# Kernel tuning notes

Hardware: AMD Instinct MI355X
Metric: run time of the kernel (lower is better)

Reference implementation:

```python
import jax, jax.numpy as jnp
import numpy as np

ATTN_C = 32
HEADS = 8
MSA_C = 256


def setup_inputs() -> dict:
    key = jax.random.key(0)
    ks = jax.random.split(key, 10)
    B, S, R, C = 1, 256, 384, MSA_C
    HC = ATTN_C * HEADS
    scale = 1.0 / np.sqrt(C)
    return {
        "msa_act": jax.random.normal(ks[0], (B, S, R, C), dtype=jnp.float32),
        "msa_mask": jnp.ones((B, S, R), dtype=jnp.float32),
        "ln_g": jnp.ones((C,), dtype=jnp.float32),
        "ln_b": jnp.zeros((C,), dtype=jnp.float32),
        "wq": jax.random.normal(ks[1], (C, HC), dtype=jnp.float32) * scale,
        "wk": jax.random.normal(ks[2], (C, HC), dtype=jnp.float32) * scale,
        "wv": jax.random.normal(ks[3], (C, HC), dtype=jnp.float32) * scale,
        "wg": jax.random.normal(ks[4], (C, HC), dtype=jnp.float32) * scale,
        "bg": jnp.zeros((HC,), dtype=jnp.float32),
        "wo": jax.random.normal(ks[5], (HC, C), dtype=jnp.float32) * (1.0 / np.sqrt(HC)),
        "bo": jnp.zeros((C,), dtype=jnp.float32),
    }


def _layernorm(x, g, b, eps=1e-5):
    mu = jnp.mean(x, axis=-1, keepdims=True)
    var = jnp.mean(jnp.square(x - mu), axis=-1, keepdims=True)
    return (x - mu) * jax.lax.rsqrt(var + eps) * g + b


def reference(msa_act, msa_mask, ln_g, ln_b, wq, wk, wv, wg, bg, wo, bo):
    H, AC = HEADS, ATTN_C
    # transpose: attend over sequence (column) axis
    x = jnp.swapaxes(msa_act, -2, -3)            # [b, R, S, C]
    mask = jnp.swapaxes(msa_mask, -1, -2)        # [b, R, S]
    bias = (1e9 * (mask - 1.0))[..., :, None, None, :]  # [b, R, 1, 1, S]
    x = _layernorm(x, ln_g, ln_b)
    shp = x.shape[:-1]
    gate = jax.nn.sigmoid((x @ wg + bg).reshape(*shp, H, AC))
    factor = 1.0 / np.sqrt(AC)
    q = (x @ wq).reshape(*shp, H, AC) * factor
    k = (x @ wk).reshape(*shp, H, AC)
    v = (x @ wv).reshape(*shp, H, AC)
    aff = jnp.einsum('brshc,brthc->brhst', q, k) + bias  # [b,R,H,S,S]
    w = jax.nn.softmax(aff, axis=-1)
    out = jnp.einsum('brhst,brthc->brshc', w, v) * gate  # [b,R,S,H,AC]
    out = out.reshape(*shp, H * AC) @ wo + bo            # [b,R,S,C]
    return jnp.swapaxes(out, -2, -3)                     # [b,S,R,C]
```

## Files before the change

kernel.cpp:

```cpp
#include <hip/hip_runtime.h>

#define S_DIM 256
#define R_DIM 384
#define C_DIM 256
#define H_DIM 8
#define AC_DIM 32
#define HC_DIM 256
#define M_DIM (S_DIM * R_DIM)

typedef __attribute__((ext_vector_type(8))) short short8;
typedef __attribute__((ext_vector_type(4))) float floatx4;

__device__ __forceinline__ unsigned short f2bf(float f) {
  unsigned u = __float_as_uint(f);
  u += 0x7FFFu + ((u >> 16) & 1u);
  return (unsigned short)(u >> 16);
}
__device__ __forceinline__ float bf2f(unsigned short s) {
  return __uint_as_float(((unsigned)s) << 16);
}
__device__ __forceinline__ unsigned packbf2(float a, float b) {
  return (unsigned)f2bf(a) | ((unsigned)f2bf(b) << 16);
}

#define GLD_LDS16(gp, lp)                                                      \
  __builtin_amdgcn_global_load_lds(                                            \
      (const __attribute__((address_space(1))) unsigned int*)(gp),             \
      (__attribute__((address_space(3))) unsigned int*)(lp), 16, 0, 0)

__global__ __launch_bounds__(256) void wcat_kernel(
    const float* __restrict__ wq, const float* __restrict__ wk,
    const float* __restrict__ wv, const float* __restrict__ wg,
    const float* __restrict__ wo, unsigned short* __restrict__ wt) {
  __shared__ float tile[64][65];
  const int n0 = blockIdx.x * 64;
  const int k0 = blockIdx.y * 64;
  const int wi = n0 >> 8;
  const float* src = (wi == 0) ? wq : (wi == 1) ? wk : (wi == 2) ? wv
                   : (wi == 3) ? wg : wo;
  const int col0 = n0 & 255;
  const int tx = threadIdx.x & 63;
  const int ty = threadIdx.x >> 6;
#pragma unroll
  for (int i = 0; i < 16; ++i) {
    int kl = ty + i * 4;
    tile[kl][tx] = src[(size_t)(k0 + kl) * 256 + col0 + tx];
  }
  __syncthreads();
#pragma unroll
  for (int i = 0; i < 16; ++i) {
    int nl = ty + i * 4;
    wt[(size_t)(n0 + nl) * 256 + k0 + tx] = f2bf(tile[tx][nl]);
  }
}

__global__ __launch_bounds__(256) void ln_kernel(
    const float* __restrict__ msa, const float* __restrict__ ln_g,
    const float* __restrict__ ln_b, unsigned short* __restrict__ xln) {
  const int p = blockIdx.x * 4 + (threadIdx.x >> 6);
  const int lane = threadIdx.x & 63;
  const float4 v = ((const float4*)(msa + (size_t)p * C_DIM))[lane];
  float s = v.x + v.y + v.z + v.w;
  float ss = v.x * v.x + v.y * v.y + v.z * v.z + v.w * v.w;
#pragma unroll
  for (int o = 1; o < 64; o <<= 1) {
    s += __shfl_xor(s, o);
    ss += __shfl_xor(ss, o);
  }
  const float mu = s * (1.0f / C_DIM);
  const float rstd = rsqrtf(ss * (1.0f / C_DIM) - mu * mu + 1e-5f);
  const float4 g = ((const float4*)ln_g)[lane];
  const float4 b = ((const float4*)ln_b)[lane];
  const int sq = p / R_DIM;
  const int r = p - sq * R_DIM;
  const size_t m = (size_t)r * S_DIM + sq;
  ushort4 o;
  o.x = f2bf((v.x - mu) * rstd * g.x + b.x);
  o.y = f2bf((v.y - mu) * rstd * g.y + b.y);
  o.z = f2bf((v.z - mu) * rstd * g.z + b.z);
  o.w = f2bf((v.w - mu) * rstd * g.w + b.w);
  *(ushort4*)(xln + m * C_DIM + lane * 4) = o;
}

#define EPI_S 136

__global__ __launch_bounds__(256, 3) void proj_kernel(
    const unsigned short* __restrict__ xln, const unsigned short* __restrict__ wt,
    const float* __restrict__ bg, unsigned short* __restrict__ q_ws,
    unsigned short* __restrict__ k_ws, unsigned short* __restrict__ v_ws,
    unsigned short* __restrict__ g_ws) {
  __shared__ __align__(16) unsigned short As[8 * 512];
  __shared__ __align__(16) unsigned short Bs[8 * 512];
  __shared__ __align__(16) unsigned short Epi[128 * EPI_S];

  const int bid = blockIdx.x;
  const int orig = (bid & 7) * 768 + (bid >> 3);
  const int n0 = (orig & 7) << 7;
  const int m0 = (orig >> 3) << 7;

  const int tid = threadIdx.x;
  const int wave = tid >> 6, lane = tid & 63;
  const int qd = lane >> 4, lm = lane & 15;
  const int wm = (wave & 1) * 64, wn = (wave >> 1) * 64;

  const int ga0 = wave * 2, ga1 = wave * 2 + 1;
  const unsigned short* agp0 = xln + (size_t)(m0 + ga0 * 16 + lm) * 256 + qd * 8;
  const unsigned short* agp1 = xln + (size_t)(m0 + ga1 * 16 + lm) * 256 + qd * 8;
  const unsigned short* bgp0 = wt + (size_t)(n0 + ga0 * 16 + lm) * 256 + qd * 8;
  const unsigned short* bgp1 = wt + (size_t)(n0 + ga1 * 16 + lm) * 256 + qd * 8;
  unsigned short* lA0 = &As[ga0 * 512];
  unsigned short* lA1 = &As[ga1 * 512];
  unsigned short* lB0 = &Bs[ga0 * 512];
  unsigned short* lB1 = &Bs[ga1 * 512];

  floatx4 acc[4][4];
#pragma unroll
  for (int i = 0; i < 4; ++i)
#pragma unroll
    for (int j = 0; j < 4; ++j) acc[i][j] = (floatx4){0.f, 0.f, 0.f, 0.f};

  for (int k0 = 0; k0 < 256; k0 += 32) {
    GLD_LDS16(agp0 + k0, lA0);
    GLD_LDS16(agp1 + k0, lA1);
    GLD_LDS16(bgp0 + k0, lB0);
    GLD_LDS16(bgp1 + k0, lB1);
    __syncthreads();
    short8 af[4], bf[4];
#pragma unroll
    for (int t = 0; t < 4; ++t) {
      af[t] = *(const short8*)((const char*)As + (size_t)(wm / 16 + t) * 1024 + lane * 16);
      bf[t] = *(const short8*)((const char*)Bs + (size_t)(wn / 16 + t) * 1024 + lane * 16);
    }
#pragma unroll
    for (int tm = 0; tm < 4; ++tm)
#pragma unroll
      for (int tn = 0; tn < 4; ++tn)
        acc[tm][tn] =
            __builtin_amdgcn_mfma_f32_16x16x32_bf16(af[tm], bf[tn], acc[tm][tn], 0, 0, 0);
    __syncthreads();
  }

  const int wi = n0 >> 8;
  const int cb = n0 & 255;
#pragma unroll
  for (int tm = 0; tm < 4; ++tm)
#pragma unroll
    for (int tn = 0; tn < 4; ++tn) {
      float bgv = 0.0f;
      if (wi == 3) bgv = bg[cb + wn + tn * 16 + lm];
#pragma unroll
      for (int rg = 0; rg < 4; ++rg) {
        const int lr = wm + tm * 16 + qd * 4 + rg;
        const int lc = wn + tn * 16 + lm;
        const float val = acc[tm][tn][rg];
        unsigned short o;
        if (wi == 0) o = f2bf(val * 0.17677669529663689f);
        else if (wi == 3) o = f2bf(1.0f / (1.0f + __expf(-(val + bgv))));
        else o = f2bf(val);
        Epi[lr * EPI_S + lc] = o;
      }
    }
  __syncthreads();
  unsigned short* dst = (wi == 0) ? q_ws : (wi == 1) ? k_ws
                      : (wi == 2) ? v_ws : g_ws;
#pragma unroll
  for (int p = 0; p < 8; ++p) {
    const int lr = (p >> 1) * 32 + (tid >> 3);
    const int lc = (p & 1) * 64 + (tid & 7) * 8;
    short8 v8 = *(const short8*)&Epi[lr * EPI_S + lc];
    *(short8*)(dst + (size_t)(m0 + lr) * 256 + cb + lc) = v8;
  }
}

#define PSTRIDE 40
#define VSTRIDE 264

__global__ __launch_bounds__(256) void attn_kernel(
    const unsigned short* __restrict__ q_ws, const unsigned short* __restrict__ k_ws,
    const unsigned short* __restrict__ v_ws, const unsigned short* __restrict__ g_ws,
    const float* __restrict__ mask, unsigned short* __restrict__ ctx_ws) {
  __shared__ __align__(16) unsigned short V_lds[32 * VSTRIDE];
  __shared__ __align__(16) unsigned short P_lds[4 * 16 * PSTRIDE];
  __shared__ float Bias[S_DIM];

  const int r = blockIdx.x;
  const int h = blockIdx.y;
  const int tid = threadIdx.x;
  const int wave = tid >> 6, lane = tid & 63;
  const int qd = lane >> 4, lm = lane & 15;
  const int qw = wave * 64;

  const size_t rS = (size_t)r * S_DIM;
  const int hb = h * AC_DIM;

  {
    const int s = tid;
    const unsigned short* vp = v_ws + (rS + s) * HC_DIM + hb;
    const int pos = (s & ~31) + ((s & 15) * 2) + ((s >> 4) & 1);
    uint4 u0 = *(const uint4*)(vp);
    uint4 u1 = *(const uint4*)(vp + 8);
    uint4 u2 = *(const uint4*)(vp + 16);
    uint4 u3 = *(const uint4*)(vp + 24);
    const unsigned w[16] = {u0.x, u0.y, u0.z, u0.w, u1.x, u1.y, u1.z, u1.w,
                            u2.x, u2.y, u2.z, u2.w, u3.x, u3.y, u3.z, u3.w};
#pragma unroll
    for (int d2 = 0; d2 < 16; ++d2) {
      V_lds[(d2 * 2 + 0) * VSTRIDE + pos] = (unsigned short)(w[d2] & 0xFFFF);
      V_lds[(d2 * 2 + 1) * VSTRIDE + pos] = (unsigned short)(w[d2] >> 16);
    }
    Bias[s] = 1e9f * (mask[(size_t)s * R_DIM + r] - 1.0f);
  }

  short8 qf[4];
#pragma unroll
  for (int qi = 0; qi < 4; ++qi)
    qf[qi] = *(const short8*)(q_ws + (rS + qw + qi * 16 + lm) * HC_DIM + hb + qd * 8);

  float m_st[4][4], l_st[4][4];
  floatx4 oacc[4][2];
#pragma unroll
  for (int qi = 0; qi < 4; ++qi) {
#pragma unroll
    for (int rg = 0; rg < 4; ++rg) {
      m_st[qi][rg] = -1e30f;
      l_st[qi][rg] = 0.0f;
    }
    oacc[qi][0] = (floatx4){0.f, 0.f, 0.f, 0.f};
    oacc[qi][1] = (floatx4){0.f, 0.f, 0.f, 0.f};
  }

  __syncthreads();

  unsigned short* Pw = &P_lds[wave * 16 * PSTRIDE];
  const floatx4 zero4 = (floatx4){0.f, 0.f, 0.f, 0.f};

  for (int ch = 0; ch < 8; ++ch) {
    const int kb = ch * 32;
    const float b0 = Bias[kb + lm];
    const float b1 = Bias[kb + 16 + lm];
    short8 kf0 = *(const short8*)(k_ws + (rS + kb + lm) * HC_DIM + hb + qd * 8);
    short8 kf1 = *(const short8*)(k_ws + (rS + kb + 16 + lm) * HC_DIM + hb + qd * 8);
    short8 vf0 = *(const short8*)&V_lds[lm * VSTRIDE + kb + qd * 8];
    short8 vf1 = *(const short8*)&V_lds[(16 + lm) * VSTRIDE + kb + qd * 8];

#pragma unroll
    for (int qi = 0; qi < 4; ++qi) {
      floatx4 s0 = __builtin_amdgcn_mfma_f32_16x16x32_bf16(qf[qi], kf0, zero4, 0, 0, 0);
      floatx4 s1 = __builtin_amdgcn_mfma_f32_16x16x32_bf16(qf[qi], kf1, zero4, 0, 0, 0);
      unsigned pw[4];
#pragma unroll
      for (int rg = 0; rg < 4; ++rg) {
        float a0 = s0[rg] + b0;
        float a1 = s1[rg] + b1;
        float t = fmaxf(a0, a1);
        t = fmaxf(t, __shfl_xor(t, 1));
        t = fmaxf(t, __shfl_xor(t, 2));
        t = fmaxf(t, __shfl_xor(t, 4));
        t = fmaxf(t, __shfl_xor(t, 8));
        float mold = m_st[qi][rg];
        float mnew = fmaxf(mold, t);
        float alpha = __expf(mold - mnew);
        float p0 = __expf(a0 - mnew);
        float p1 = __expf(a1 - mnew);
        float rs = p0 + p1;
        rs += __shfl_xor(rs, 1);
        rs += __shfl_xor(rs, 2);
        rs += __shfl_xor(rs, 4);
        rs += __shfl_xor(rs, 8);
        l_st[qi][rg] = l_st[qi][rg] * alpha + rs;
        m_st[qi][rg] = mnew;
        oacc[qi][0][rg] *= alpha;
        oacc[qi][1][rg] *= alpha;
        pw[rg] = packbf2(p0, p1);
      }
      unsigned* pbase = (unsigned*)Pw;
#pragma unroll
      for (int rg = 0; rg < 4; ++rg)
        pbase[((qd * 4 + rg) * PSTRIDE) / 2 + lm] = pw[rg];
      short8 pa = *(const short8*)&Pw[lm * PSTRIDE + qd * 8];
      oacc[qi][0] = __builtin_amdgcn_mfma_f32_16x16x32_bf16(pa, vf0, oacc[qi][0], 0, 0, 0);
      oacc[qi][1] = __builtin_amdgcn_mfma_f32_16x16x32_bf16(pa, vf1, oacc[qi][1], 0, 0, 0);
    }
  }

#pragma unroll
  for (int qi = 0; qi < 4; ++qi) {
#pragma unroll
    for (int rg = 0; rg < 4; ++rg) {
      const float inv = 1.0f / l_st[qi][rg];
      const int row = qw + qi * 16 + qd * 4 + rg;
      const size_t base = (rS + row) * HC_DIM + hb;
      float o0 = oacc[qi][0][rg] * inv * bf2f(g_ws[base + lm]);
      float o1 = oacc[qi][1][rg] * inv * bf2f(g_ws[base + 16 + lm]);
      ctx_ws[base + lm] = f2bf(o0);
      ctx_ws[base + 16 + lm] = f2bf(o1);
    }
  }
}

#define EPF_S 132

__global__ __launch_bounds__(256, 3) void out_kernel(
    const unsigned short* __restrict__ ctx, const unsigned short* __restrict__ wot,
    const float* __restrict__ bo, float* __restrict__ out) {
  __shared__ __align__(16) unsigned short As[8 * 512];
  __shared__ __align__(16) unsigned short Bs[8 * 512];
  __shared__ __align__(16) float Epif[64 * EPF_S];

  const int bid = blockIdx.x;
  const int orig = (bid & 7) * 192 + (bid >> 3);
  const int n0 = (orig & 1) << 7;
  const int m0 = (orig >> 1) << 7;

  const int tid = threadIdx.x;
  const int wave = tid >> 6, lane = tid & 63;
  const int qd = lane >> 4, lm = lane & 15;
  const int wm = (wave & 1) * 64, wn = (wave >> 1) * 64;

  const int ga0 = wave * 2, ga1 = wave * 2 + 1;
  const unsigned short* agp0 = ctx + (size_t)(m0 + ga0 * 16 + lm) * 256 + qd * 8;
  const unsigned short* agp1 = ctx + (size_t)(m0 + ga1 * 16 + lm) * 256 + qd * 8;
  const unsigned short* bgp0 = wot + (size_t)(n0 + ga0 * 16 + lm) * 256 + qd * 8;
  const unsigned short* bgp1 = wot + (size_t)(n0 + ga1 * 16 + lm) * 256 + qd * 8;
  unsigned short* lA0 = &As[ga0 * 512];
  unsigned short* lA1 = &As[ga1 * 512];
  unsigned short* lB0 = &Bs[ga0 * 512];
  unsigned short* lB1 = &Bs[ga1 * 512];

  floatx4 acc[4][4];
#pragma unroll
  for (int i = 0; i < 4; ++i)
#pragma unroll
    for (int j = 0; j < 4; ++j) acc[i][j] = (floatx4){0.f, 0.f, 0.f, 0.f};

  for (int k0 = 0; k0 < 256; k0 += 32) {
    GLD_LDS16(agp0 + k0, lA0);
    GLD_LDS16(agp1 + k0, lA1);
    GLD_LDS16(bgp0 + k0, lB0);
    GLD_LDS16(bgp1 + k0, lB1);
    __syncthreads();
    short8 af[4], bf[4];
#pragma unroll
    for (int t = 0; t < 4; ++t) {
      af[t] = *(const short8*)((const char*)As + (size_t)(wm / 16 + t) * 1024 + lane * 16);
      bf[t] = *(const short8*)((const char*)Bs + (size_t)(wn / 16 + t) * 1024 + lane * 16);
    }
#pragma unroll
    for (int tm = 0; tm < 4; ++tm)
#pragma unroll
      for (int tn = 0; tn < 4; ++tn)
        acc[tm][tn] =
            __builtin_amdgcn_mfma_f32_16x16x32_bf16(af[tm], bf[tn], acc[tm][tn], 0, 0, 0);
    __syncthreads();
  }

#pragma unroll
  for (int h = 0; h < 2; ++h) {
    __syncthreads();
    if (wm == h * 64) {
#pragma unroll
      for (int tm = 0; tm < 4; ++tm)
#pragma unroll
        for (int tn = 0; tn < 4; ++tn) {
          const float bov = bo[n0 + wn + tn * 16 + lm];
#pragma unroll
          for (int rg = 0; rg < 4; ++rg) {
            const int lr = tm * 16 + qd * 4 + rg;
            const int lc = wn + tn * 16 + lm;
            Epif[lr * EPF_S + lc] = acc[tm][tn][rg] + bov;
          }
        }
    }
    __syncthreads();
#pragma unroll
    for (int p = 0; p < 8; ++p) {
      const int lr = p * 8 + (tid >> 5);
      const int lc = (tid & 31) * 4;
      float4 vv = *(const float4*)&Epif[lr * EPF_S + lc];
      const int m = m0 + h * 64 + lr;
      const int rr = m >> 8, sc = m & 255;
      *(float4*)(out + ((size_t)sc * R_DIM + rr) * C_DIM + n0 + lc) = vv;
    }
  }
}

extern "C" void kernel_launch(void* const* d_in, const int* in_sizes, int n_in,
                              void* d_out, int out_size, void* d_ws, size_t ws_size,
                              hipStream_t stream) {
  const float* msa = (const float*)d_in[0];
  const float* mask = (const float*)d_in[1];
  const float* ln_g = (const float*)d_in[2];
  const float* ln_b = (const float*)d_in[3];
  const float* wq = (const float*)d_in[4];
  const float* wk = (const float*)d_in[5];
  const float* wv = (const float*)d_in[6];
  const float* wg = (const float*)d_in[7];
  const float* bg = (const float*)d_in[8];
  const float* wo = (const float*)d_in[9];
  const float* bo = (const float*)d_in[10];
  float* out = (float*)d_out;

  unsigned short* wt = (unsigned short*)d_ws;
  unsigned short* xln = wt + (size_t)1280 * 256;
  unsigned short* q_ws = xln + (size_t)M_DIM * 256;
  unsigned short* k_ws = q_ws + (size_t)M_DIM * 256;
  unsigned short* v_ws = k_ws + (size_t)M_DIM * 256;
  unsigned short* g_ws = v_ws + (size_t)M_DIM * 256;
  unsigned short* ctx_ws = xln;
  unsigned short* wot = wt + (size_t)1024 * 256;

  hipLaunchKernelGGL(wcat_kernel, dim3(20, 4), dim3(256), 0, stream,
                     wq, wk, wv, wg, wo, wt);
  hipLaunchKernelGGL(ln_kernel, dim3(M_DIM / 4), dim3(256), 0, stream,
                     msa, ln_g, ln_b, xln);
  hipLaunchKernelGGL(proj_kernel, dim3(6144), dim3(256), 0, stream,
                     xln, wt, bg, q_ws, k_ws, v_ws, g_ws);
  hipLaunchKernelGGL(attn_kernel, dim3(R_DIM, H_DIM), dim3(256), 0, stream,
                     q_ws, k_ws, v_ws, g_ws, mask, ctx_ws);
  hipLaunchKernelGGL(out_kernel, dim3(1536), dim3(256), 0, stream,
                     ctx_ws, wot, bo, out);
}
```

Measured before the change: 551.8 us.

## Transpose score MFMA so softmax reduces per lane, with lazy max rescaling

Measured after the change: 460.2 us. 1.2x faster.

```diff
diff --git a/kernel.cpp b/kernel.cpp
--- a/kernel.cpp
+++ b/kernel.cpp
@@ -10,6 +10,7 @@
 
 typedef __attribute__((ext_vector_type(8))) short short8;
 typedef __attribute__((ext_vector_type(4))) float floatx4;
+typedef __attribute__((ext_vector_type(2))) unsigned int uint2v;
 
 __device__ __forceinline__ unsigned short f2bf(float f) {
   unsigned u = __float_as_uint(f);
@@ -196,7 +197,6 @@
   {
     const int s = tid;
     const unsigned short* vp = v_ws + (rS + s) * HC_DIM + hb;
-    const int pos = (s & ~31) + ((s & 15) * 2) + ((s >> 4) & 1);
     uint4 u0 = *(const uint4*)(vp);
     uint4 u1 = *(const uint4*)(vp + 8);
     uint4 u2 = *(const uint4*)(vp + 16);
@@ -205,8 +205,8 @@
                             u2.x, u2.y, u2.z, u2.w, u3.x, u3.y, u3.z, u3.w};
 #pragma unroll
     for (int d2 = 0; d2 < 16; ++d2) {
-      V_lds[(d2 * 2 + 0) * VSTRIDE + pos] = (unsigned short)(w[d2] & 0xFFFF);
-      V_lds[(d2 * 2 + 1) * VSTRIDE + pos] = (unsigned short)(w[d2] >> 16);
+      V_lds[(d2 * 2 + 0) * VSTRIDE + s] = (unsigned short)(w[d2] & 0xFFFF);
+      V_lds[(d2 * 2 + 1) * VSTRIDE + s] = (unsigned short)(w[d2] >> 16);
     }
     Bias[s] = 1e9f * (mask[(size_t)s * R_DIM + r] - 1.0f);
   }
@@ -216,15 +216,12 @@
   for (int qi = 0; qi < 4; ++qi)
     qf[qi] = *(const short8*)(q_ws + (rS + qw + qi * 16 + lm) * HC_DIM + hb + qd * 8);
 
-  float m_st[4][4], l_st[4][4];
+  float m_q[4], l_q[4];
   floatx4 oacc[4][2];
 #pragma unroll
   for (int qi = 0; qi < 4; ++qi) {
-#pragma unroll
-    for (int rg = 0; rg < 4; ++rg) {
-      m_st[qi][rg] = -1e30f;
-      l_st[qi][rg] = 0.0f;
-    }
+    m_q[qi] = -1e30f;
+    l_q[qi] = 0.0f;
     oacc[qi][0] = (floatx4){0.f, 0.f, 0.f, 0.f};
     oacc[qi][1] = (floatx4){0.f, 0.f, 0.f, 0.f};
   }
@@ -233,50 +230,57 @@
 
   unsigned short* Pw = &P_lds[wave * 16 * PSTRIDE];
   const floatx4 zero4 = (floatx4){0.f, 0.f, 0.f, 0.f};
+  const int qd4 = qd * 4;
 
   for (int ch = 0; ch < 8; ++ch) {
     const int kb = ch * 32;
-    const float b0 = Bias[kb + lm];
-    const float b1 = Bias[kb + 16 + lm];
     short8 kf0 = *(const short8*)(k_ws + (rS + kb + lm) * HC_DIM + hb + qd * 8);
     short8 kf1 = *(const short8*)(k_ws + (rS + kb + 16 + lm) * HC_DIM + hb + qd * 8);
     short8 vf0 = *(const short8*)&V_lds[lm * VSTRIDE + kb + qd * 8];
     short8 vf1 = *(const short8*)&V_lds[(16 + lm) * VSTRIDE + kb + qd * 8];
+    const floatx4 bl = *(const floatx4*)&Bias[kb + qd4];
+    const floatx4 bh = *(const floatx4*)&Bias[kb + 16 + qd4];
 
 #pragma unroll
     for (int qi = 0; qi < 4; ++qi) {
-      floatx4 s0 = __builtin_amdgcn_mfma_f32_16x16x32_bf16(qf[qi], kf0, zero4, 0, 0, 0);
-      floatx4 s1 = __builtin_amdgcn_mfma_f32_16x16x32_bf16(qf[qi], kf1, zero4, 0, 0, 0);
-      unsigned pw[4];
+      floatx4 s0 = __builtin_amdgcn_mfma_f32_16x16x32_bf16(kf0, qf[qi], zero4, 0, 0, 0);
+      floatx4 s1 = __builtin_amdgcn_mfma_f32_16x16x32_bf16(kf1, qf[qi], zero4, 0, 0, 0);
+      s0 += bl;
+      s1 += bh;
+      float t = fmaxf(fmaxf(fmaxf(s0[0], s0[1]), fmaxf(s0[2], s0[3])),
+                      fmaxf(fmaxf(s1[0], s1[1]), fmaxf(s1[2], s1[3])));
+      t = fmaxf(t, __shfl_xor(t, 16));
+      t = fmaxf(t, __shfl_xor(t, 32));
+      float mold = m_q[qi];
+      if (__any(t > mold + 8.0f)) {
+        const float mnew = fmaxf(mold, t);
+        const float alpha = __expf(mold - mnew);
+#pragma unroll
+        for (int rg = 0; rg < 4; ++rg) {
+          const float arg = __shfl(alpha, qd4 + rg);
+          oacc[qi][0][rg] *= arg;
+          oacc[qi][1][rg] *= arg;
+        }
+        l_q[qi] *= alpha;
+        m_q[qi] = mnew;
+        mold = mnew;
+      }
+      floatx4 p0, p1;
 #pragma unroll
       for (int rg = 0; rg < 4; ++rg) {
-        float a0 = s0[rg] + b0;
-        float a1 = s1[rg] + b1;
-        float t = fmaxf(a0, a1);
-        t = fmaxf(t, __shfl_xor(t, 1));
-        t = fmaxf(t, __shfl_xor(t, 2));
-        t = fmaxf(t, __shfl_xor(t, 4));
-        t = fmaxf(t, __shfl_xor(t, 8));
-        float mold = m_st[qi][rg];
-        float mnew = fmaxf(mold, t);
-        float alpha = __expf(mold - mnew);
-        float p0 = __expf(a0 - mnew);
-        float p1 = __expf(a1 - mnew);
-        float rs = p0 + p1;
-        rs += __shfl_xor(rs, 1);
-        rs += __shfl_xor(rs, 2);
-        rs += __shfl_xor(rs, 4);
-        rs += __shfl_xor(rs, 8);
-        l_st[qi][rg] = l_st[qi][rg] * alpha + rs;
-        m_st[qi][rg] = mnew;
-        oacc[qi][0][rg] *= alpha;
-        oacc[qi][1][rg] *= alpha;
-        pw[rg] = packbf2(p0, p1);
+        p0[rg] = __expf(s0[rg] - mold);
+        p1[rg] = __expf(s1[rg] - mold);
       }
-      unsigned* pbase = (unsigned*)Pw;
-#pragma unroll
-      for (int rg = 0; rg < 4; ++rg)
-        pbase[((qd * 4 + rg) * PSTRIDE) / 2 + lm] = pw[rg];
+      float rs = ((p0[0] + p0[1]) + (p0[2] + p0[3])) +
+                 ((p1[0] + p1[1]) + (p1[2] + p1[3]));
+      rs += __shfl_xor(rs, 16);
+      rs += __shfl_xor(rs, 32);
+      l_q[qi] += rs;
+      unsigned* prow = (unsigned*)&Pw[lm * PSTRIDE];
+      uint2v lo = {packbf2(p0[0], p0[1]), packbf2(p0[2], p0[3])};
+      uint2v hi = {packbf2(p1[0], p1[1]), packbf2(p1[2], p1[3])};
+      *(uint2v*)&prow[qd * 2] = lo;
+      *(uint2v*)&prow[8 + qd * 2] = hi;
       short8 pa = *(const short8*)&Pw[lm * PSTRIDE + qd * 8];
       oacc[qi][0] = __builtin_amdgcn_mfma_f32_16x16x32_bf16(pa, vf0, oacc[qi][0], 0, 0, 0);
       oacc[qi][1] = __builtin_amdgcn_mfma_f32_16x16x32_bf16(pa, vf1, oacc[qi][1], 0, 0, 0);
@@ -285,10 +289,11 @@
 
 #pragma unroll
   for (int qi = 0; qi < 4; ++qi) {
+    const float lq = l_q[qi];
 #pragma unroll
     for (int rg = 0; rg < 4; ++rg) {
-      const float inv = 1.0f / l_st[qi][rg];
-      const int row = qw + qi * 16 + qd * 4 + rg;
+      const float inv = 1.0f / __shfl(lq, qd4 + rg);
+      const int row = qw + qi * 16 + qd4 + rg;
       const size_t base = (rS + row) * HC_DIM + hb;
       float o0 = oacc[qi][0][rg] * inv * bf2f(g_ws[base + lm]);
       float o1 = oacc[qi][1][rg] * inv * bf2f(g_ws[base + 16 + lm]);
```
